# Optimization experiments

Hardware: AMD Instinct MI355X
Metric: run time of the kernel (lower is better)

Reference implementation:

```python
import jax, jax.numpy as jnp
import numpy as np

HIDDEN = 512
NUM_HEADS = 8
HEAD_DIM = HIDDEN // NUM_HEADS


def setup_inputs() -> dict:
    key = jax.random.key(0)
    k1, k2 = jax.random.split(key)
    x = jax.random.normal(k1, (2, 2048, HIDDEN), dtype=jnp.float32)
    # torch Linear(h, 3h, bias=False): weight shape [3h, h], y = x @ W.T
    W_qkv = jax.random.normal(k2, (3 * HIDDEN, HIDDEN), dtype=jnp.float32) * (HIDDEN ** -0.5)
    return {"x": x, "W_qkv": W_qkv}


def reference(x, W_qkv):
    B, S, h = x.shape
    H, d = NUM_HEADS, HEAD_DIM
    temperature = (1.0 / d) ** 0.5  # sqrt(1/head_dim)
    qkv = x @ W_qkv.T  # [B, S, 3h]
    # Original chunks 3h into H pieces of size 3d (per-head interleaved QKV),
    # stacks on dim=1 -> [B, H, S, 3d], then splits into Q, K, V.
    qkv = qkv.reshape(B, S, H, 3 * d).transpose(0, 2, 1, 3)  # [B, H, S, 3d]
    q, k, v = jnp.split(qkv, 3, axis=-1)  # each [B, H, S, d]
    scores = jnp.einsum("bhqd,bhkd->bhqk", q * temperature, k)  # [B, H, S, S]
    # dropout is inference no-op; mask branch in original is a dead assignment
    w = jax.nn.softmax(scores, axis=-1)
    out = jnp.einsum("bhqk,bhkd->bhqd", w, v)  # [B, H, S, d]
    # torch.cat over heads on last dim == transpose back + merge heads
    return out.transpose(0, 2, 1, 3).reshape(B, S, h)
```

## Files before the change

kernel.cpp:

```cpp
#include <hip/hip_runtime.h>
#include <stdint.h>

#define HD 512
#define NH 8
#define DH 64
#define SEQ 2048
#define BATCH 2
#define M_TOTAL (BATCH*SEQ)
#define N_QKV (3*HD)
#define K_DIM HD

typedef short bf16x8 __attribute__((ext_vector_type(8)));
typedef float f32x4 __attribute__((ext_vector_type(4)));
typedef uint32_t u32x2 __attribute__((ext_vector_type(2)));

#define QSCALE 0.18033688011112042f

__device__ __forceinline__ uint16_t f2bf(float f) {
  union { float f; uint32_t u; } v; v.f = f;
  uint32_t u = v.u;
  return (uint16_t)((u + 0x7FFFu + ((u >> 16) & 1u)) >> 16);
}

__device__ __forceinline__ void gload_lds16(const void* g, void* l) {
  __builtin_amdgcn_global_load_lds(
      (const __attribute__((address_space(1))) void*)g,
      (__attribute__((address_space(3))) void*)l,
      16, 0, 0);
}

__global__ void convert_f32_to_bf16(const float* __restrict__ in,
                                    uint16_t* __restrict__ out, int n4) {
  int i = blockIdx.x * blockDim.x + threadIdx.x;
  if (i < n4) {
    float4 v = reinterpret_cast<const float4*>(in)[i];
    ushort4 o;
    o.x = f2bf(v.x); o.y = f2bf(v.y); o.z = f2bf(v.z); o.w = f2bf(v.w);
    reinterpret_cast<ushort4*>(out)[i] = o;
  }
}

#define BM 128
#define BN 128
#define BK 64
#define NKT (K_DIM / BK)

__global__ __launch_bounds__(256)
void qkv_gemm(const uint16_t* __restrict__ A,
              const uint16_t* __restrict__ Bw,
              uint16_t* __restrict__ C,
              uint16_t* __restrict__ Vt) {
  __shared__ __align__(16) uint16_t As[2][BM * BK];
  __shared__ __align__(16) uint16_t Bs[2][BM * BK];

  const int t = threadIdx.x;
  const int lane = t & 63;
  const int w = t >> 6;
  const int wr = w >> 1, wc = w & 1;
  const int l15 = lane & 15, l4 = lane >> 4;
  const int m0 = blockIdx.y * BM;
  const int n0 = blockIdx.x * BN;

  f32x4 acc[4][4] = {};

  auto stage = [&](int kt, int buf) {
#pragma unroll
    for (int i = 0; i < 4; ++i) {
      int idx = t + 256 * i;
      int row = idx >> 3, slot = idx & 7;
      int src = slot ^ (row & 7);
      gload_lds16(A + (size_t)(m0 + row) * K_DIM + kt * BK + src * 8,
                  (char*)As[buf] + idx * 16);
      gload_lds16(Bw + (size_t)(n0 + row) * K_DIM + kt * BK + src * 8,
                  (char*)Bs[buf] + idx * 16);
    }
  };

  stage(0, 0);
  for (int kt = 0; kt < NKT; ++kt) {
    __syncthreads();
    if (kt + 1 < NKT) stage(kt + 1, (kt + 1) & 1);
    const char* Ab = (const char*)As[kt & 1];
    const char* Bb = (const char*)Bs[kt & 1];
#pragma unroll
    for (int kk = 0; kk < 2; ++kk) {
      bf16x8 af[4], bfr[4];
#pragma unroll
      for (int i = 0; i < 4; ++i) {
        int rowa = wr * 64 + i * 16 + l15;
        int sa = (kk * 4 + l4) ^ (rowa & 7);
        af[i] = *reinterpret_cast<const bf16x8*>(Ab + rowa * 128 + sa * 16);
        int rowb = wc * 64 + i * 16 + l15;
        int sb = (kk * 4 + l4) ^ (rowb & 7);
        bfr[i] = *reinterpret_cast<const bf16x8*>(Bb + rowb * 128 + sb * 16);
      }
      __builtin_amdgcn_s_setprio(1);
#pragma unroll
      for (int i = 0; i < 4; ++i)
#pragma unroll
        for (int j = 0; j < 4; ++j)
          acc[i][j] = __builtin_amdgcn_mfma_f32_16x16x32_bf16(af[i], bfr[j], acc[i][j], 0, 0, 0);
      __builtin_amdgcn_s_setprio(0);
    }
  }

#pragma unroll
  for (int i = 0; i < 4; ++i) {
    int row = m0 + wr * 64 + i * 16 + l4 * 4;
#pragma unroll
    for (int j = 0; j < 4; ++j) {
      int colb = n0 + wc * 64 + j * 16;
      int col = colb + l15;
      int cls = (colb % 192) >> 6;
      if (cls == 2) {
        int h = col / 192;
        int d = col - h * 192 - 128;
        int b = row >> 11;
        int s = row & (SEQ - 1);
        ushort4 o;
        o.x = f2bf(acc[i][j][0]); o.y = f2bf(acc[i][j][1]);
        o.z = f2bf(acc[i][j][2]); o.w = f2bf(acc[i][j][3]);
        *reinterpret_cast<ushort4*>(Vt + ((size_t)(b * NH + h) * DH + d) * SEQ + s) = o;
      } else {
        float sc = (cls == 0) ? QSCALE : 1.0f;
#pragma unroll
        for (int jj = 0; jj < 4; ++jj)
          C[(size_t)(row + jj) * N_QKV + col] = f2bf(acc[i][j][jj] * sc);
      }
    }
  }
}

#define NT (SEQ / 64)

__global__ __launch_bounds__(256)
void attn(const uint16_t* __restrict__ qkv, const uint16_t* __restrict__ VtG,
          float* __restrict__ out) {
  __shared__ __align__(16) uint16_t Kt[2][64 * 64];
  __shared__ __align__(16) uint16_t Vt[2][64 * 64];
  __shared__ __align__(16) uint16_t Pl[4][16 * 64];

  const int t = threadIdx.x;
  const int lane = t & 63;
  const int w = t >> 6;
  const int l15 = lane & 15, l4 = lane >> 4;
  const int bh = blockIdx.x;
  const int b = bh >> 3, h = bh & 7;
  const int q0 = blockIdx.y * 64;
  const int qw = q0 + w * 16;

  bf16x8 qf[2];
  {
    const uint16_t* qp = qkv + (size_t)(b * SEQ + qw + l15) * N_QKV + h * 192;
#pragma unroll
    for (int kk = 0; kk < 2; ++kk)
      qf[kk] = *reinterpret_cast<const bf16x8*>(qp + kk * 32 + l4 * 8);
  }

  const uint16_t* kgbase = qkv + (size_t)b * SEQ * N_QKV + h * 192 + 64;
  const uint16_t* vgbase = VtG + (size_t)bh * DH * SEQ;

  auto stage = [&](int ti, int buf) {
    int s0 = ti * 64;
#pragma unroll
    for (int i = 0; i < 2; ++i) {
      int idx = t + 256 * i;
      int row = idx >> 3, slot = idx & 7;
      int src = slot ^ (row & 7);
      gload_lds16(kgbase + (size_t)(s0 + row) * N_QKV + src * 8,
                  (char*)Kt[buf] + idx * 16);
      gload_lds16(vgbase + (size_t)row * SEQ + s0 + src * 8,
                  (char*)Vt[buf] + idx * 16);
    }
  };

  f32x4 o[4] = {};
  float mrow = -1e30f, lrow = 0.0f;

  stage(0, 0);
  for (int ti = 0; ti < NT; ++ti) {
    __syncthreads();
    if (ti + 1 < NT) stage(ti + 1, (ti + 1) & 1);
    const char* Kb = (const char*)Kt[ti & 1];
    const char* Vb = (const char*)Vt[ti & 1];

    f32x4 s[4] = {};
#pragma unroll
    for (int c = 0; c < 4; ++c) {
#pragma unroll
      for (int kk = 0; kk < 2; ++kk) {
        int row = c * 16 + l15;
        int sl = (kk * 4 + l4) ^ (row & 7);
        bf16x8 kf = *reinterpret_cast<const bf16x8*>(Kb + row * 128 + sl * 16);
        __builtin_amdgcn_s_setprio(1);
        s[c] = __builtin_amdgcn_mfma_f32_16x16x32_bf16(kf, qf[kk], s[c], 0, 0, 0);
        __builtin_amdgcn_s_setprio(0);
      }
    }

    float vmax = s[0][0];
#pragma unroll
    for (int c = 0; c < 4; ++c)
#pragma unroll
      for (int jj = 0; jj < 4; ++jj) vmax = fmaxf(vmax, s[c][jj]);
    vmax = fmaxf(vmax, __shfl_xor(vmax, 16, 64));
    vmax = fmaxf(vmax, __shfl_xor(vmax, 32, 64));

    if (!__all(vmax - mrow <= 11.0f)) {
      float mn = fmaxf(mrow, vmax);
      float sc;
      float darg = mrow - mn;
      asm("v_exp_f32 %0, %1" : "=v"(sc) : "v"(darg));
      mrow = mn;
      float sr[4];
#pragma unroll
      for (int jj = 0; jj < 4; ++jj) sr[jj] = __shfl(sc, l4 * 4 + jj, 64);
#pragma unroll
      for (int f = 0; f < 4; ++f)
#pragma unroll
        for (int jj = 0; jj < 4; ++jj) o[f][jj] *= sr[jj];
      lrow *= sc;
    }

    float p[16];
#pragma unroll
    for (int c = 0; c < 4; ++c)
#pragma unroll
      for (int jj = 0; jj < 4; ++jj) {
        float arg = s[c][jj] - mrow;
        float e;
        asm("v_exp_f32 %0, %1" : "=v"(e) : "v"(arg));
        p[c * 4 + jj] = e;
      }
    float a0 = (p[0] + p[1]) + (p[2] + p[3]);
    float a1 = (p[4] + p[5]) + (p[6] + p[7]);
    float a2 = (p[8] + p[9]) + (p[10] + p[11]);
    float a3 = (p[12] + p[13]) + (p[14] + p[15]);
    float tsum = (a0 + a1) + (a2 + a3);
    tsum += __shfl_xor(tsum, 16, 64);
    tsum += __shfl_xor(tsum, 32, 64);
    lrow += tsum;

#pragma unroll
    for (int c = 0; c < 4; ++c) {
      uint32_t lo, hi;
      asm("v_cvt_pk_bf16_f32 %0, %1, %2" : "=v"(lo) : "v"(p[c * 4 + 0]), "v"(p[c * 4 + 1]));
      asm("v_cvt_pk_bf16_f32 %0, %1, %2" : "=v"(hi) : "v"(p[c * 4 + 2]), "v"(p[c * 4 + 3]));
      int slot = 2 * c + (l4 >> 1);
      int byteoff = l15 * 128 + ((slot ^ (l15 & 7)) * 16) + (l4 & 1) * 8;
      u32x2 pk; pk.x = lo; pk.y = hi;
      *reinterpret_cast<u32x2*>((char*)Pl[w] + byteoff) = pk;
    }

#pragma unroll
    for (int kk = 0; kk < 2; ++kk) {
      int sp = (kk * 4 + l4) ^ (l15 & 7);
      bf16x8 pa = *reinterpret_cast<const bf16x8*>((const char*)Pl[w] + l15 * 128 + sp * 16);
      __builtin_amdgcn_s_setprio(1);
#pragma unroll
      for (int f = 0; f < 4; ++f) {
        int d = f * 16 + l15;
        int sv = (kk * 4 + l4) ^ (d & 7);
        bf16x8 vf = *reinterpret_cast<const bf16x8*>(Vb + d * 128 + sv * 16);
        o[f] = __builtin_amdgcn_mfma_f32_16x16x32_bf16(pa, vf, o[f], 0, 0, 0);
      }
      __builtin_amdgcn_s_setprio(0);
    }
  }

  float lr[4];
#pragma unroll
  for (int jj = 0; jj < 4; ++jj) lr[jj] = __shfl(lrow, l4 * 4 + jj, 64);
#pragma unroll
  for (int f = 0; f < 4; ++f) {
    int d = f * 16 + l15;
#pragma unroll
    for (int jj = 0; jj < 4; ++jj) {
      int q = qw + l4 * 4 + jj;
      out[(size_t)(b * SEQ + q) * HD + h * 64 + d] = o[f][jj] / lr[jj];
    }
  }
}

extern "C" void kernel_launch(void* const* d_in, const int* in_sizes, int n_in,
                              void* d_out, int out_size, void* d_ws, size_t ws_size,
                              hipStream_t stream) {
  const float* x = (const float*)d_in[0];
  const float* Wq = (const float*)d_in[1];
  float* out = (float*)d_out;

  uint16_t* xb = (uint16_t*)d_ws;
  uint16_t* Wb = xb + (size_t)M_TOTAL * K_DIM;
  uint16_t* qkv = Wb + (size_t)N_QKV * K_DIM;
  uint16_t* vtg = qkv + (size_t)M_TOTAL * N_QKV;

  convert_f32_to_bf16<<<(M_TOTAL * K_DIM / 4 + 255) / 256, 256, 0, stream>>>(
      x, xb, M_TOTAL * K_DIM / 4);
  convert_f32_to_bf16<<<(N_QKV * K_DIM / 4 + 255) / 256, 256, 0, stream>>>(
      Wq, Wb, N_QKV * K_DIM / 4);

  dim3 g1(N_QKV / BN, M_TOTAL / BM);
  qkv_gemm<<<g1, 256, 0, stream>>>(xb, Wb, qkv, vtg);

  dim3 g2(BATCH * NH, SEQ / 64);
  attn<<<g2, 256, 0, stream>>>(qkv, vtg, out);
}
```

Baseline: 125.3 us.

## Split attention KV range across two blocks, add combine kernel, remap GEMM tiles

The attention grid gains a z dimension that splits the key sequence in two. Each half writes unnormalised partial outputs plus its running max and sum to workspace, and a new combine kernel merges them with a log-sum-exp rescale. This doubles the number of blocks (512 to 1024) to fill more CUs, at the cost of extra fp32 partial traffic and an extra launch. The QKV GEMM also remaps block ids across 8 groups (likely for XCD locality), stages the V transpose through LDS so it writes coalesced 16-byte rows, and moves setprio to wrap whole MFMA groups.

```diff
diff --git a/kernel.cpp b/kernel.cpp
--- a/kernel.cpp
+++ b/kernel.cpp
@@ -13,6 +13,7 @@
 typedef short bf16x8 __attribute__((ext_vector_type(8)));
 typedef float f32x4 __attribute__((ext_vector_type(4)));
 typedef uint32_t u32x2 __attribute__((ext_vector_type(2)));
+typedef uint32_t u32x4 __attribute__((ext_vector_type(4)));
 
 #define QSCALE 0.18033688011112042f
 
@@ -58,8 +59,14 @@
   const int w = t >> 6;
   const int wr = w >> 1, wc = w & 1;
   const int l15 = lane & 15, l4 = lane >> 4;
-  const int m0 = blockIdx.y * BM;
-  const int n0 = blockIdx.x * BN;
+
+  const int nbx = gridDim.x;
+  const int nwg = nbx * gridDim.y;
+  const int cpx = nwg >> 3;
+  int id = blockIdx.y * nbx + blockIdx.x;
+  int wid = (id & 7) * cpx + (id >> 3);
+  const int m0 = (wid / nbx) * BM;
+  const int n0 = (wid % nbx) * BN;
 
   f32x4 acc[4][4] = {};
 
@@ -94,35 +101,52 @@
         int sb = (kk * 4 + l4) ^ (rowb & 7);
         bfr[i] = *reinterpret_cast<const bf16x8*>(Bb + rowb * 128 + sb * 16);
       }
-      __builtin_amdgcn_s_setprio(1);
 #pragma unroll
       for (int i = 0; i < 4; ++i)
 #pragma unroll
         for (int j = 0; j < 4; ++j)
           acc[i][j] = __builtin_amdgcn_mfma_f32_16x16x32_bf16(af[i], bfr[j], acc[i][j], 0, 0, 0);
-      __builtin_amdgcn_s_setprio(0);
-    }
-  }
-
-#pragma unroll
-  for (int i = 0; i < 4; ++i) {
-    int row = m0 + wr * 64 + i * 16 + l4 * 4;
-#pragma unroll
-    for (int j = 0; j < 4; ++j) {
-      int colb = n0 + wc * 64 + j * 16;
-      int col = colb + l15;
-      int cls = (colb % 192) >> 6;
-      if (cls == 2) {
-        int h = col / 192;
-        int d = col - h * 192 - 128;
-        int b = row >> 11;
-        int s = row & (SEQ - 1);
-        ushort4 o;
-        o.x = f2bf(acc[i][j][0]); o.y = f2bf(acc[i][j][1]);
-        o.z = f2bf(acc[i][j][2]); o.w = f2bf(acc[i][j][3]);
-        *reinterpret_cast<ushort4*>(Vt + ((size_t)(b * NH + h) * DH + d) * SEQ + s) = o;
-      } else {
-        float sc = (cls == 0) ? QSCALE : 1.0f;
+    }
+  }
+
+  const int colw = n0 + wc * 64;
+  const bool isv = ((colw % 192) == 128);
+  __syncthreads();
+
+  if (isv) {
+    char* tb = (char*)As + w * 8192;
+#pragma unroll
+    for (int i = 0; i < 4; ++i)
+#pragma unroll
+      for (int j = 0; j < 4; ++j) {
+        uint32_t lo, hi;
+        asm("v_cvt_pk_bf16_f32 %0, %1, %2" : "=v"(lo) : "v"(acc[i][j][0]), "v"(acc[i][j][1]));
+        asm("v_cvt_pk_bf16_f32 %0, %1, %2" : "=v"(hi) : "v"(acc[i][j][2]), "v"(acc[i][j][3]));
+        int dl = j * 16 + l15;
+        int byteoff = dl * 128 + (((i * 2 + (l4 >> 1)) ^ (dl & 7)) * 16) + (l4 & 1) * 8;
+        u32x2 pk; pk.x = lo; pk.y = hi;
+        *reinterpret_cast<u32x2*>(tb + byteoff) = pk;
+      }
+    int h = colw / 192;
+    int b = (m0 + wr * 64) >> 11;
+    int sbase = (m0 + wr * 64) & (SEQ - 1);
+    uint16_t* vbase = Vt + (size_t)(b * NH + h) * DH * SEQ + sbase + (lane & 7) * 8;
+#pragma unroll
+    for (int p = 0; p < 8; ++p) {
+      int dl = p * 8 + (lane >> 3);
+      u32x4 rv = *reinterpret_cast<const u32x4*>(
+          tb + dl * 128 + (((lane & 7) ^ (dl & 7)) * 16));
+      *reinterpret_cast<u32x4*>(vbase + (size_t)dl * SEQ) = rv;
+    }
+  } else {
+#pragma unroll
+    for (int i = 0; i < 4; ++i) {
+      int row = m0 + wr * 64 + i * 16 + l4 * 4;
+#pragma unroll
+      for (int j = 0; j < 4; ++j) {
+        int colb = colw + j * 16;
+        int col = colb + l15;
+        float sc = (((colb % 192) >> 6) == 0) ? QSCALE : 1.0f;
 #pragma unroll
         for (int jj = 0; jj < 4; ++jj)
           C[(size_t)(row + jj) * N_QKV + col] = f2bf(acc[i][j][jj] * sc);
@@ -135,7 +159,8 @@
 
 __global__ __launch_bounds__(256)
 void attn(const uint16_t* __restrict__ qkv, const uint16_t* __restrict__ VtG,
-          float* __restrict__ out) {
+          float* __restrict__ Po,
+          float2* __restrict__ Pml) {
   __shared__ __align__(16) uint16_t Kt[2][64 * 64];
   __shared__ __align__(16) uint16_t Vt[2][64 * 64];
   __shared__ __align__(16) uint16_t Pl[4][16 * 64];
@@ -148,6 +173,9 @@
   const int b = bh >> 3, h = bh & 7;
   const int q0 = blockIdx.y * 64;
   const int qw = q0 + w * 16;
+  const int half = blockIdx.z;
+  const int tph = NT / gridDim.z;
+  const int t0 = half * tph;
 
   bf16x8 qf[2];
   {
@@ -177,14 +205,16 @@
   f32x4 o[4] = {};
   float mrow = -1e30f, lrow = 0.0f;
 
-  stage(0, 0);
-  for (int ti = 0; ti < NT; ++ti) {
+  stage(t0, 0);
+  for (int rel = 0; rel < tph; ++rel) {
+    int ti = t0 + rel;
     __syncthreads();
-    if (ti + 1 < NT) stage(ti + 1, (ti + 1) & 1);
-    const char* Kb = (const char*)Kt[ti & 1];
-    const char* Vb = (const char*)Vt[ti & 1];
+    if (rel + 1 < tph) stage(ti + 1, (rel + 1) & 1);
+    const char* Kb = (const char*)Kt[rel & 1];
+    const char* Vb = (const char*)Vt[rel & 1];
 
     f32x4 s[4] = {};
+    __builtin_amdgcn_s_setprio(1);
 #pragma unroll
     for (int c = 0; c < 4; ++c) {
 #pragma unroll
@@ -192,11 +222,10 @@
         int row = c * 16 + l15;
         int sl = (kk * 4 + l4) ^ (row & 7);
         bf16x8 kf = *reinterpret_cast<const bf16x8*>(Kb + row * 128 + sl * 16);
-        __builtin_amdgcn_s_setprio(1);
         s[c] = __builtin_amdgcn_mfma_f32_16x16x32_bf16(kf, qf[kk], s[c], 0, 0, 0);
-        __builtin_amdgcn_s_setprio(0);
-      }
-    }
+      }
+    }
+    __builtin_amdgcn_s_setprio(0);
 
     float vmax = s[0][0];
 #pragma unroll
@@ -252,11 +281,11 @@
       *reinterpret_cast<u32x2*>((char*)Pl[w] + byteoff) = pk;
     }
 
+    __builtin_amdgcn_s_setprio(1);
 #pragma unroll
     for (int kk = 0; kk < 2; ++kk) {
       int sp = (kk * 4 + l4) ^ (l15 & 7);
       bf16x8 pa = *reinterpret_cast<const bf16x8*>((const char*)Pl[w] + l15 * 128 + sp * 16);
-      __builtin_amdgcn_s_setprio(1);
 #pragma unroll
       for (int f = 0; f < 4; ++f) {
         int d = f * 16 + l15;
@@ -264,22 +293,54 @@
         bf16x8 vf = *reinterpret_cast<const bf16x8*>(Vb + d * 128 + sv * 16);
         o[f] = __builtin_amdgcn_mfma_f32_16x16x32_bf16(pa, vf, o[f], 0, 0, 0);
       }
-      __builtin_amdgcn_s_setprio(0);
-    }
-  }
-
-  float lr[4];
-#pragma unroll
-  for (int jj = 0; jj < 4; ++jj) lr[jj] = __shfl(lrow, l4 * 4 + jj, 64);
+    }
+    __builtin_amdgcn_s_setprio(0);
+  }
+
+  float* pob = Po + ((size_t)(half * 16 + bh) * SEQ) * DH;
 #pragma unroll
   for (int f = 0; f < 4; ++f) {
     int d = f * 16 + l15;
 #pragma unroll
     for (int jj = 0; jj < 4; ++jj) {
       int q = qw + l4 * 4 + jj;
-      out[(size_t)(b * SEQ + q) * HD + h * 64 + d] = o[f][jj] / lr[jj];
-    }
-  }
+      pob[(size_t)q * DH + d] = o[f][jj];
+    }
+  }
+  if (lane < 16) {
+    float2 ml; ml.x = mrow; ml.y = lrow;
+    Pml[(size_t)(half * 16 + bh) * SEQ + qw + lane] = ml;
+  }
+}
+
+__global__ __launch_bounds__(256)
+void attn_combine(const float* __restrict__ Po, const float2* __restrict__ Pml,
+                  float* __restrict__ out, int nsplit) {
+  int idx = blockIdx.x * 256 + threadIdx.x;
+  int d4 = idx & 15;
+  int q = (idx >> 4) & (SEQ - 1);
+  int bh = idx >> 15;
+  int b = bh >> 3, h = bh & 7;
+
+  float2 ml0 = Pml[(size_t)bh * SEQ + q];
+  f32x4 o0 = *reinterpret_cast<const f32x4*>(
+      Po + ((size_t)bh * SEQ + q) * DH + d4 * 4);
+  f32x4 res;
+  if (nsplit == 2) {
+    float2 ml1 = Pml[(size_t)(16 + bh) * SEQ + q];
+    f32x4 o1 = *reinterpret_cast<const f32x4*>(
+        Po + ((size_t)(16 + bh) * SEQ + q) * DH + d4 * 4);
+    float m = fmaxf(ml0.x, ml1.x);
+    float a0 = exp2f(ml0.x - m), a1 = exp2f(ml1.x - m);
+    float rden = 1.0f / (ml0.y * a0 + ml1.y * a1);
+#pragma unroll
+    for (int i = 0; i < 4; ++i) res[i] = (o0[i] * a0 + o1[i] * a1) * rden;
+  } else {
+    float rden = 1.0f / ml0.y;
+#pragma unroll
+    for (int i = 0; i < 4; ++i) res[i] = o0[i] * rden;
+  }
+  *reinterpret_cast<f32x4*>(out + ((size_t)(b * SEQ + q) * HD) + h * 64 + d4 * 4) = res;
 }
 
 extern "C" void kernel_launch(void* const* d_in, const int* in_sizes, int n_in,
@@ -293,6 +354,10 @@
   uint16_t* Wb = xb + (size_t)M_TOTAL * K_DIM;
   uint16_t* qkv = Wb + (size_t)N_QKV * K_DIM;
   uint16_t* vtg = qkv + (size_t)M_TOTAL * N_QKV;
+  float* Po = (float*)(vtg + (size_t)16 * DH * SEQ);
+  float2* Pml = (float2*)(Po + (size_t)2 * 16 * SEQ * DH);
+  size_t need2 = (char*)(Pml + (size_t)2 * 16 * SEQ) - (char*)d_ws;
+  int nsplit = (ws_size >= need2) ? 2 : 1;
 
   convert_f32_to_bf16<<<(M_TOTAL * K_DIM / 4 + 255) / 256, 256, 0, stream>>>(
       x, xb, M_TOTAL * K_DIM / 4);
@@ -302,6 +367,8 @@
   dim3 g1(N_QKV / BN, M_TOTAL / BM);
   qkv_gemm<<<g1, 256, 0, stream>>>(xb, Wb, qkv, vtg);
 
-  dim3 g2(BATCH * NH, SEQ / 64);
-  attn<<<g2, 256, 0, stream>>>(qkv, vtg, out);
-}
+  dim3 g2(BATCH * NH, SEQ / 64, nsplit);
+  attn<<<g2, 256, 0, stream>>>(qkv, vtg, Po, Pml);
+
+  attn_combine<<<(16 * SEQ * 16) / 256, 256, 0, stream>>>(Po, Pml, out, nsplit);
+}
```

Result: faster. 114.6 us (-8.6%).
